# Performance work log

Measured on AMD Instinct MI355X. Metric: run time of the kernel, lower is better.

## Reference

```python
import jax, jax.numpy as jnp
import numpy as np
import math

B, SEQ, PRED, F, DM, NH, DFF, S, DMARK = 16, 336, 96, 7, 512, 8, 2048, 16, 5
EL, DL = 2, 1
DH = DM // NH


def _pe(max_len, d):
    pos = np.arange(max_len)[:, None].astype(np.float32)
    div = np.exp(np.arange(0, d, 2).astype(np.float32) * (-math.log(10000.0) / d))
    pe = np.zeros((max_len, d), np.float32)
    pe[:, 0::2] = np.sin(pos * div)
    pe[:, 1::2] = np.cos(pos * div)
    return jnp.asarray(pe)


def _make_tao():
    t = np.ones((S, S), np.float32)
    t[:, 0] = 0.0
    t[:, -1] = 0.0
    t[1] *= -1.0
    t[0] = 0.0
    t[0, 0] = 1.0
    t[2:, 1:-1] = np.eye(S - 2, dtype=np.float32)
    return jnp.asarray(t)


PE = _pe(2000, DM)
TAO = _make_tao()
ZVEC = jnp.zeros((S,), jnp.float32).at[:2].set(1.0)
MASK = jnp.triu(jnp.full((PRED, PRED), -1e9, jnp.float32), k=1)  # causal additive mask


def _ln(x, w, b, eps=1e-5):
    m = x.mean(-1, keepdims=True)
    v = ((x - m) ** 2).mean(-1, keepdims=True)
    return (x - m) * jax.lax.rsqrt(v + eps) * w + b


def _mha(q_in, kv_in, qkv_w, qkv_b, ow, ob, mask=None):
    wq, wk, wv = jnp.split(qkv_w, 3, axis=0)
    bq, bk, bv = jnp.split(qkv_b, 3, axis=0)

    def proj(x, w, bb):
        y = x @ w.T + bb  # [B, T, DM]
        return y.reshape(y.shape[0], y.shape[1], NH, DH).transpose(0, 2, 1, 3)

    q, k, v = proj(q_in, wq, bq), proj(kv_in, wk, bk), proj(kv_in, wv, bv)
    s = jnp.einsum('bhqd,bhkd->bhqk', q, k) / math.sqrt(DH)
    if mask is not None:
        s = s + mask
    a = jax.nn.softmax(s, axis=-1)
    o = jnp.einsum('bhqk,bhkd->bhqd', a, v)
    o = o.transpose(0, 2, 1, 3).reshape(q_in.shape)
    return o @ ow.T + ob


def _per_feature(xe, xd, eqw, eqb, eow, eob, el1w, el1b, el2w, el2b,
                 ef1w, ef1b, ef2w, ef2b, elw, elb,
                 dsqw, dsqb, dsow, dsob, dcqw, dcqb, dcow, dcob,
                 dl1w, dl1b, dl2w, dl2b, dl3w, dl3b, df1w, df1b, df2w, df2b):
    # post-norm TransformerEncoder (relu FFN), eval mode (no dropout)
    h = xe
    for l in range(EL):
        h = _ln(h + _mha(h, h, eqw[l], eqb[l], eow[l], eob[l]), el1w[l], el1b[l])
        ff = jax.nn.relu(h @ ef1w[l].T + ef1b[l]) @ ef2w[l].T + ef2b[l]
        h = _ln(h + ff, el2w[l], el2b[l])
    # encoder_linear maps time axis seqlen -> prelen
    mem = jnp.einsum('bsd,ps->bpd', h, elw) + elb[None, :, None]
    t = xd
    for l in range(DL):
        t = _ln(t + _mha(t, t, dsqw[l], dsqb[l], dsow[l], dsob[l], MASK), dl1w[l], dl1b[l])
        t = _ln(t + _mha(t, mem, dcqw[l], dcqb[l], dcow[l], dcob[l]), dl2w[l], dl2b[l])
        ff = jax.nn.relu(t @ df1w[l].T + df1b[l]) @ df2w[l].T + df2b[l]
        t = _ln(t + ff, dl3w[l], dl3b[l])
    return t


_vfeat = jax.vmap(_per_feature, in_axes=(1, 1) + (0,) * 32, out_axes=1)


def setup_inputs():
    key = jax.random.key(0)
    ks = iter(jax.random.split(key, 64))

    def rn(shape, s=0.05):
        return jax.random.normal(next(ks), shape, jnp.float32) * s

    return {
        'batch_x': rn((B, SEQ, F), 1.0),
        'batch_x_mark': rn((B, SEQ, DMARK - 1), 1.0),
        'batch_y': rn((B, PRED, F), 1.0),
        'batch_y_mark': rn((B, PRED, DMARK - 1), 1.0),
        'w_in': rn((DM, DMARK)), 'b_in': rn((DM,)),
        'w_co': rn((DM, DMARK - 1)), 'b_co': rn((DM,)),
        'eqw': rn((F, EL, 3 * DM, DM)), 'eqb': rn((F, EL, 3 * DM)),
        'eow': rn((F, EL, DM, DM)), 'eob': rn((F, EL, DM)),
        'el1w': jnp.ones((F, EL, DM)), 'el1b': jnp.zeros((F, EL, DM)),
        'el2w': jnp.ones((F, EL, DM)), 'el2b': jnp.zeros((F, EL, DM)),
        'ef1w': rn((F, EL, DFF, DM)), 'ef1b': rn((F, EL, DFF)),
        'ef2w': rn((F, EL, DM, DFF)), 'ef2b': rn((F, EL, DM)),
        'elw': rn((F, PRED, SEQ)), 'elb': rn((F, PRED)),
        'dsqw': rn((F, DL, 3 * DM, DM)), 'dsqb': rn((F, DL, 3 * DM)),
        'dsow': rn((F, DL, DM, DM)), 'dsob': rn((F, DL, DM)),
        'dcqw': rn((F, DL, 3 * DM, DM)), 'dcqb': rn((F, DL, 3 * DM)),
        'dcow': rn((F, DL, DM, DM)), 'dcob': rn((F, DL, DM)),
        'dl1w': jnp.ones((F, DL, DM)), 'dl1b': jnp.zeros((F, DL, DM)),
        'dl2w': jnp.ones((F, DL, DM)), 'dl2b': jnp.zeros((F, DL, DM)),
        'dl3w': jnp.ones((F, DL, DM)), 'dl3b': jnp.zeros((F, DL, DM)),
        'df1w': rn((F, DL, DFF, DM)), 'df1b': rn((F, DL, DFF)),
        'df2w': rn((F, DL, DM, DFF)), 'df2b': rn((F, DL, DM)),
        'wc': rn((S, DM)), 'bc': rn((S,)),
        'ws': rn((1, DM)), 'bs': rn((1,)),
    }


def reference(batch_x, batch_x_mark, batch_y, batch_y_mark,
              w_in, b_in, w_co, b_co,
              eqw, eqb, eow, eob, el1w, el1b, el2w, el2b,
              ef1w, ef1b, ef2w, ef2b, elw, elb,
              dsqw, dsqb, dsow, dsob, dcqw, dcqb, dcow, dcob,
              dl1w, dl1b, dl2w, dl2b, dl3w, dl3b, df1w, df1b, df2w, df2b,
              wc, bc, ws, bs):
    Bsz = batch_x.shape[0]
    # time marks are shared across features -> broadcast instead of concat loop
    hist = jnp.concatenate(
        [batch_x[..., None],
         jnp.broadcast_to(batch_x_mark[:, :, None, :], (Bsz, SEQ, F, DMARK - 1))], axis=-1)
    fut = jnp.broadcast_to(batch_y_mark[:, -PRED:, None, :], (Bsz, PRED, F, DMARK - 1))
    hist = hist.transpose(0, 2, 1, 3)  # [B, F, SEQ, DMARK]
    fut = fut.transpose(0, 2, 1, 3)    # [B, F, PRED, DMARK-1]
    xe = hist @ w_in.T + b_in + PE[:SEQ]
    xd = fut @ w_co.T + b_co + PE[:PRED]
    dec = _vfeat(xe, xd, eqw, eqb, eow, eob, el1w, el1b, el2w, el2b,
                 ef1w, ef1b, ef2w, ef2b, elw, elb,
                 dsqw, dsqb, dsow, dsob, dcqw, dcqb, dcow, dcob,
                 dl1w, dl1b, dl2w, dl2b, dl3w, dl3b, df1w, df1b, df2w, df2b)
    # g_c = Linear + Hardsigmoid; g_s = Linear + Softplus
    c = jnp.clip((jnp.einsum('bfpd,sd->bfps', dec, wc) + bc) / 6.0 + 0.5, 0.0, 1.0)
    sig = jax.nn.softplus(jnp.einsum('bfpd,d->bfp', dec, ws[0]) + bs[0])
    # linear state recurrence a = TAO @ a + c, y = z^T a, scanned over prediction days
    a0 = c[:, :, 0]                      # [B, F, S] (torch initializes a with day-0 g_c)
    cs = jnp.moveaxis(c, 2, 0)           # [PRED, B, F, S]
    ss = jnp.moveaxis(sig, 2, 0)         # [PRED, B, F]

    def step(a, xs):
        cd, sd = xs
        a = jnp.einsum('ij,bfj->bfi', TAO, a) + cd
        return a, jnp.einsum('s,bfs->bf', ZVEC, a) + sd

    _, ys = jax.lax.scan(step, a0, (cs, ss))
    return jnp.transpose(ys, (1, 0, 2))  # [B, PRED, F]
```

## Files before the change

kernel.cpp:

```cpp
#include <hip/hip_runtime.h>

typedef unsigned short u16;
typedef unsigned int   u32;
typedef __attribute__((ext_vector_type(8))) short short8;
typedef __attribute__((ext_vector_type(4))) float f32x4;

#define DEV static __device__ __forceinline__

DEV float bf2f(u16 u) { return __uint_as_float(((u32)u) << 16); }
DEV u16 f2bf(float f) {
  u32 u = __float_as_uint(f);
  return (u16)((u + 0x7fffu + ((u >> 16) & 1u)) >> 16);
}

#define GLD16(gp, lp) __builtin_amdgcn_global_load_lds( \
    (__attribute__((address_space(1))) u32*)(gp),       \
    (__attribute__((address_space(3))) u32*)(lp), 16, 0, 0)

__global__ __launch_bounds__(512, 2) void gemm_bf16(
    const u16* __restrict__ A, const u16* __restrict__ Bw, u16* __restrict__ C,
    const float* __restrict__ bias, int M, int N, int K,
    long sAz, long sBz, long sCz, long sBiasZ, int relu)
{
  __shared__ __align__(16) u16 Asm[2][256 * 64];
  __shared__ __align__(16) u16 Bsm[2][256 * 64];

  int gx = (int)gridDim.x, gy = (int)gridDim.y;
  int nwg = gx * gy * (int)gridDim.z;
  int orig = (int)blockIdx.x + gx * ((int)blockIdx.y + gy * (int)blockIdx.z);
  int q = nwg >> 3, r = nwg & 7;
  int xcd = orig & 7, pos = orig >> 3;
  int lg_id = (xcd < r) ? (xcd * (q + 1) + pos) : (r * (q + 1) + (xcd - r) * q + pos);
  int bz = lg_id / (gx * gy);
  int rem = lg_id - bz * (gx * gy);
  int by = rem / gx, bx = rem - by * gx;

  A += (size_t)bz * sAz; Bw += (size_t)bz * sBz; C += (size_t)bz * sCz; bias += (size_t)bz * sBiasZ;
  int tileM = bx * 256, tileN = by * 256;
  int tid = threadIdx.x, wave = tid >> 6, lane = tid & 63;
  int lr = lane & 15, lgp = lane >> 4;
  int wm = (wave >> 2) * 128;
  int wn = (wave & 3) * 64;

  const int NT = K >> 6;

  auto STAGE = [&](int b, int t) {
    int kb = t * 64;
    #pragma unroll
    for (int i = 0; i < 4; i++) {
      int gi = i * 512 + wave * 64 + lane;
      int row = gi >> 3, g = gi & 7;
      int gsw = (g ^ (row & 7)) * 8;
      GLD16(A + (size_t)(tileM + row) * K + kb + gsw, &Asm[b][(size_t)gi * 8]);
      GLD16(Bw + (size_t)(tileN + row) * K + kb + gsw, &Bsm[b][(size_t)gi * 8]);
    }
  };

  f32x4 acc[8][4] = {};

  STAGE(0, 0);
  if (NT > 1) STAGE(1, 1);

  for (int t = 0; t < NT; ++t) {
    int cur = t & 1;
    if (t + 1 < NT) asm volatile("s_waitcnt vmcnt(8)" ::: "memory");
    else            asm volatile("s_waitcnt vmcnt(0)" ::: "memory");
    asm volatile("s_barrier" ::: "memory");

    const u16* Ab = Asm[cur];
    const u16* Bb = Bsm[cur];
    #pragma unroll
    for (int ks = 0; ks < 2; ++ks) {
      short8 bfr[4], afr[8];
      #pragma unroll
      for (int n = 0; n < 4; ++n) {
        int row = wn + n * 16 + lr;
        bfr[n] = *(const short8*)(Bb + row * 64 + (((ks * 4 + lgp) ^ (row & 7)) * 8));
      }
      #pragma unroll
      for (int m = 0; m < 8; ++m) {
        int row = wm + m * 16 + lr;
        afr[m] = *(const short8*)(Ab + row * 64 + (((ks * 4 + lgp) ^ (row & 7)) * 8));
      }
      __builtin_amdgcn_s_setprio(1);
      #pragma unroll
      for (int m = 0; m < 8; ++m)
        #pragma unroll
        for (int n = 0; n < 4; ++n)
          acc[m][n] = __builtin_amdgcn_mfma_f32_16x16x32_bf16(afr[m], bfr[n], acc[m][n], 0, 0, 0);
      __builtin_amdgcn_s_setprio(0);
    }
    asm volatile("s_waitcnt lgkmcnt(0)" ::: "memory");
    asm volatile("s_barrier" ::: "memory");
    if (t + 2 < NT) STAGE(cur, t + 2);
  }

  #pragma unroll
  for (int n = 0; n < 4; ++n) {
    int ncol = tileN + wn + n * 16 + lr;
    float bb = bias[ncol];
    #pragma unroll
    for (int m = 0; m < 8; ++m) {
      int mrow = tileM + wm + m * 16 + lgp * 4;
      #pragma unroll
      for (int rr = 0; rr < 4; ++rr) {
        float v = acc[m][n][rr] + bb;
        if (relu) v = fmaxf(v, 0.f);
        C[(size_t)(mrow + rr) * N + ncol] = f2bf(v);
      }
    }
  }
}

__global__ void cvt_w_kernel(const float* __restrict__ src, u16* __restrict__ dst,
                             long n_per_f, long f_stride, long total4)
{
  long i = (long)blockIdx.x * blockDim.x + threadIdx.x;
  long step = (long)gridDim.x * blockDim.x;
  for (; i < total4; i += step) {
    long e = i * 4;
    long f = e / n_per_f; long r = e - f * n_per_f;
    float4 v = *(const float4*)(src + f * f_stride + r);
    *(ushort4*)(dst + e) = make_ushort4(f2bf(v.x), f2bf(v.y), f2bf(v.z), f2bf(v.w));
  }
}

__global__ __launch_bounds__(128) void embed_enc_k(
    const float* __restrict__ x, const float* __restrict__ mark,
    const float* __restrict__ w_in, const float* __restrict__ b_in,
    u16* __restrict__ hb)
{
  int row = blockIdx.x;
  int f = row / 5376; int rem = row - f * 5376; int b = rem / 336; int s = rem - b * 336;
  int bsix = b * 336 + s;
  float v0 = x[(size_t)bsix * 7 + f];
  float m0 = mark[(size_t)bsix * 4 + 0], m1 = mark[(size_t)bsix * 4 + 1];
  float m2 = mark[(size_t)bsix * 4 + 2], m3 = mark[(size_t)bsix * 4 + 3];
  int d0 = threadIdx.x * 4;
  u16 ob[4];
  #pragma unroll
  for (int c = 0; c < 4; c++) {
    int d = d0 + c;
    const float* w = w_in + d * 5;
    float val = w[0] * v0 + w[1] * m0 + w[2] * m1 + w[3] * m2 + w[4] * m3 + b_in[d];
    int i = d >> 1;
    float dv = expf((float)i * -0.0359778920778f);
    float arg = (float)s * dv;
    val += (d & 1) ? cosf(arg) : sinf(arg);
    ob[c] = f2bf(val);
  }
  *(ushort4*)(hb + (size_t)row * 512 + d0) = make_ushort4(ob[0], ob[1], ob[2], ob[3]);
}

__global__ __launch_bounds__(128) void embed_dec_k(
    const float* __restrict__ ymark, const float* __restrict__ w_co,
    const float* __restrict__ b_co, u16* __restrict__ tb)
{
  int row = blockIdx.x;
  int f = row / 1536; int rem = row - f * 1536; int b = rem / 96; int pp = rem - b * 96;
  int bp = b * 96 + pp;
  float m0 = ymark[(size_t)bp * 4 + 0], m1 = ymark[(size_t)bp * 4 + 1];
  float m2 = ymark[(size_t)bp * 4 + 2], m3 = ymark[(size_t)bp * 4 + 3];
  int d0 = threadIdx.x * 4;
  u16 ob[4];
  #pragma unroll
  for (int c = 0; c < 4; c++) {
    int d = d0 + c;
    const float* w = w_co + d * 4;
    float val = w[0] * m0 + w[1] * m1 + w[2] * m2 + w[3] * m3 + b_co[d];
    int i = d >> 1;
    float dv = expf((float)i * -0.0359778920778f);
    float arg = (float)pp * dv;
    val += (d & 1) ? cosf(arg) : sinf(arg);
    ob[c] = f2bf(val);
  }
  *(ushort4*)(tb + (size_t)row * 512 + d0) = make_ushort4(ob[0], ob[1], ob[2], ob[3]);
}

template<int LK>
__global__ __launch_bounds__(256) void attn_mfma(
    const u16* __restrict__ q, const u16* __restrict__ k, const u16* __restrict__ v,
    u16* __restrict__ out, int Lq, int qstride, int kvstride, int causal)
{
  constexpr int NKT = LK / 16;
  constexpr int NKS = (LK + 31) / 32;
  constexpr int KPAD = NKS * 32;
  constexpr int VSTR = 360;

  __shared__ __align__(16) u16 KsS[LK * 64];
  __shared__ __align__(16) u16 VtS[64 * VSTR];
  __shared__ __align__(16) u16 PWS[4][16 * VSTR];

  int hh = blockIdx.x, fb = blockIdx.y;
  int tid = threadIdx.x, wave = tid >> 6, lane = tid & 63;

  const u16* qp = q + (size_t)fb * Lq * qstride + hh * 64;
  const u16* kp = k + (size_t)fb * LK * kvstride + hh * 64;
  const u16* vp = v + (size_t)fb * LK * kvstride + hh * 64;

  {
    int r = (lane >> 3), s = lane & 7;
    for (int r0 = wave * 8; r0 < LK; r0 += 32) {
      int row = r0 + r;
      const u16* src = kp + (size_t)row * kvstride + ((s ^ (row & 7)) * 8);
      GLD16(src, KsS + r0 * 64 + lane * 8);
    }
  }
  for (int idx = tid; idx < LK * 8; idx += 256) {
    int kk = idx >> 3, dg = idx & 7;
    uint4 pv = *(const uint4*)(vp + (size_t)kk * kvstride + dg * 8);
    u16 e0 = (u16)pv.x, e1 = (u16)(pv.x >> 16);
    u16 e2 = (u16)pv.y, e3 = (u16)(pv.y >> 16);
    u16 e4 = (u16)pv.z, e5 = (u16)(pv.z >> 16);
    u16 e6 = (u16)pv.w, e7 = (u16)(pv.w >> 16);
    u16* col = VtS + (size_t)(dg * 8) * VSTR + kk;
    col[0 * VSTR] = e0; col[1 * VSTR] = e1; col[2 * VSTR] = e2; col[3 * VSTR] = e3;
    col[4 * VSTR] = e4; col[5 * VSTR] = e5; col[6 * VSTR] = e6; col[7 * VSTR] = e7;
  }
  if constexpr (KPAD > LK) {
    constexpr int TW = KPAD - LK;
    for (int i = tid; i < 64 * TW; i += 256)
      VtS[(i / TW) * VSTR + LK + (i % TW)] = 0;
    u16* PW = PWS[wave];
    for (int i = lane; i < 16 * TW; i += 64)
      PW[(i / TW) * VSTR + LK + (i % TW)] = 0;
  }
  __syncthreads();

  u16* PW = PWS[wave];
  int lr = lane & 15, lg = lane >> 4;
  int nqt = Lq / 16;

  for (int qt = wave; qt < nqt; qt += 4) {
    const u16* qrow = qp + (size_t)(qt * 16 + lr) * qstride + lg * 8;
    short8 qf0 = *(const short8*)(qrow);
    short8 qf1 = *(const short8*)(qrow + 32);

    f32x4 sacc[NKT];
    #pragma unroll
    for (int t = 0; t < NKT; t++) {
      int row = t * 16 + lr;
      const u16* kb = KsS + row * 64;
      short8 kf0 = *(const short8*)(kb + ((lg) ^ (row & 7)) * 8);
      short8 kf1 = *(const short8*)(kb + ((lg + 4) ^ (row & 7)) * 8);
      f32x4 s = {0.f, 0.f, 0.f, 0.f};
      s = __builtin_amdgcn_mfma_f32_16x16x32_bf16(qf0, kf0, s, 0, 0, 0);
      s = __builtin_amdgcn_mfma_f32_16x16x32_bf16(qf1, kf1, s, 0, 0, 0);
      sacc[t] = s;
    }

    float mx0 = -3e38f, mx1 = -3e38f, mx2 = -3e38f, mx3 = -3e38f;
    #pragma unroll
    for (int t = 0; t < NKT; t++) {
      int kg = t * 16 + lr;
      #pragma unroll
      for (int r = 0; r < 4; r++) {
        float val = sacc[t][r] * 0.125f;
        int qg = qt * 16 + lg * 4 + r;
        if (causal && kg > qg) val = -1e30f;
        sacc[t][r] = val;
        if (r == 0) mx0 = fmaxf(mx0, val);
        if (r == 1) mx1 = fmaxf(mx1, val);
        if (r == 2) mx2 = fmaxf(mx2, val);
        if (r == 3) mx3 = fmaxf(mx3, val);
      }
    }
    #pragma unroll
    for (int m = 1; m < 16; m <<= 1) {
      mx0 = fmaxf(mx0, __shfl_xor(mx0, m));
      mx1 = fmaxf(mx1, __shfl_xor(mx1, m));
      mx2 = fmaxf(mx2, __shfl_xor(mx2, m));
      mx3 = fmaxf(mx3, __shfl_xor(mx3, m));
    }
    float sm0 = 0.f, sm1 = 0.f, sm2 = 0.f, sm3 = 0.f;
    #pragma unroll
    for (int t = 0; t < NKT; t++) {
      float p0 = __expf(sacc[t][0] - mx0);
      float p1 = __expf(sacc[t][1] - mx1);
      float p2 = __expf(sacc[t][2] - mx2);
      float p3 = __expf(sacc[t][3] - mx3);
      sacc[t][0] = p0; sacc[t][1] = p1; sacc[t][2] = p2; sacc[t][3] = p3;
      sm0 += p0; sm1 += p1; sm2 += p2; sm3 += p3;
    }
    #pragma unroll
    for (int m = 1; m < 16; m <<= 1) {
      sm0 += __shfl_xor(sm0, m);
      sm1 += __shfl_xor(sm1, m);
      sm2 += __shfl_xor(sm2, m);
      sm3 += __shfl_xor(sm3, m);
    }
    float inv0 = 1.f / sm0, inv1 = 1.f / sm1, inv2 = 1.f / sm2, inv3 = 1.f / sm3;

    #pragma unroll
    for (int t = 0; t < NKT; t++) {
      u16* pw = PW + (size_t)(lg * 4) * VSTR + t * 16 + lr;
      pw[0 * VSTR] = f2bf(sacc[t][0]);
      pw[1 * VSTR] = f2bf(sacc[t][1]);
      pw[2 * VSTR] = f2bf(sacc[t][2]);
      pw[3 * VSTR] = f2bf(sacc[t][3]);
    }

    f32x4 oacc[4] = {};
    #pragma unroll
    for (int s = 0; s < NKS; s++) {
      short8 pf = *(const short8*)(PW + (size_t)lr * VSTR + s * 32 + lg * 8);
      #pragma unroll
      for (int j = 0; j < 4; j++) {
        short8 vf = *(const short8*)(VtS + (size_t)(j * 16 + lr) * VSTR + s * 32 + lg * 8);
        oacc[j] = __builtin_amdgcn_mfma_f32_16x16x32_bf16(pf, vf, oacc[j], 0, 0, 0);
      }
    }

    #pragma unroll
    for (int r = 0; r < 4; r++) {
      float inv = (r == 0) ? inv0 : (r == 1) ? inv1 : (r == 2) ? inv2 : inv3;
      size_t orow = (size_t)fb * Lq + qt * 16 + lg * 4 + r;
      u16* ob = out + orow * 512 + hh * 64 + lr;
      #pragma unroll
      for (int j = 0; j < 4; j++)
        ob[j * 16] = f2bf(oacc[j][r] * inv);
    }
  }
}

__global__ __launch_bounds__(128) void ln_kernel(
    u16* __restrict__ h, const u16* __restrict__ delta,
    const float* __restrict__ gamma, const float* __restrict__ beta,
    int rows_per_f, long gstride)
{
  __shared__ float red[2];
  int row = blockIdx.x;
  int f = row / rows_per_f;
  const float* g = gamma + (size_t)f * gstride;
  const float* be = beta + (size_t)f * gstride;
  int d0 = threadIdx.x * 4;
  size_t p = (size_t)row * 512 + d0;
  ushort4 hv = *(const ushort4*)(h + p);
  ushort4 dv = *(const ushort4*)(delta + p);
  float x0 = bf2f(hv.x) + bf2f(dv.x), x1 = bf2f(hv.y) + bf2f(dv.y);
  float x2 = bf2f(hv.z) + bf2f(dv.z), x3 = bf2f(hv.w) + bf2f(dv.w);
  float ssum = x0 + x1 + x2 + x3;
  #pragma unroll
  for (int m = 1; m < 64; m <<= 1) ssum += __shfl_xor(ssum, m);
  if ((threadIdx.x & 63) == 0) red[threadIdx.x >> 6] = ssum;
  __syncthreads();
  float mean = (red[0] + red[1]) * (1.f / 512.f);
  __syncthreads();
  float c0 = x0 - mean, c1 = x1 - mean, c2 = x2 - mean, c3 = x3 - mean;
  float sq = c0 * c0 + c1 * c1 + c2 * c2 + c3 * c3;
  #pragma unroll
  for (int m = 1; m < 64; m <<= 1) sq += __shfl_xor(sq, m);
  if ((threadIdx.x & 63) == 0) red[threadIdx.x >> 6] = sq;
  __syncthreads();
  float var = (red[0] + red[1]) * (1.f / 512.f);
  float rstd = rsqrtf(var + 1e-5f);
  float y0 = c0 * rstd * g[d0 + 0] + be[d0 + 0];
  float y1 = c1 * rstd * g[d0 + 1] + be[d0 + 1];
  float y2 = c2 * rstd * g[d0 + 2] + be[d0 + 2];
  float y3 = c3 * rstd * g[d0 + 3] + be[d0 + 3];
  *(ushort4*)(h + p) = make_ushort4(f2bf(y0), f2bf(y1), f2bf(y2), f2bf(y3));
}

__global__ __launch_bounds__(256) void mem_kernel(
    const u16* __restrict__ h, const float* __restrict__ elw,
    const float* __restrict__ elb, u16* __restrict__ memb)
{
  int fb = blockIdx.x; int f = fb >> 4;
  int pc = blockIdx.y;
  int d0 = threadIdx.x * 2;
  const u16* hbase = h + (size_t)fb * 336 * 512;
  const float* wbase = elw + (size_t)f * 96 * 336 + (size_t)pc * 16 * 336;
  float a0[16], a1[16];
  #pragma unroll
  for (int pp = 0; pp < 16; pp++) { a0[pp] = 0.f; a1[pp] = 0.f; }
  for (int s = 0; s < 336; s++) {
    ushort2 h2 = *(const ushort2*)(hbase + (size_t)s * 512 + d0);
    float hx = bf2f(h2.x), hy = bf2f(h2.y);
    #pragma unroll
    for (int pp = 0; pp < 16; pp++) {
      float w = wbase[pp * 336 + s];
      a0[pp] += w * hx; a1[pp] += w * hy;
    }
  }
  #pragma unroll
  for (int pp = 0; pp < 16; pp++) {
    int pidx = pc * 16 + pp;
    size_t row = (size_t)fb * 96 + pidx;
    float e = elb[f * 96 + pidx];
    *(ushort2*)(memb + row * 512 + d0) = make_ushort2(f2bf(a0[pp] + e), f2bf(a1[pp] + e));
  }
}

__global__ __launch_bounds__(64) void head_kernel(
    const u16* __restrict__ td, const float* __restrict__ wcp, const float* __restrict__ bcp,
    const float* __restrict__ wsp, const float* __restrict__ bsp,
    float* __restrict__ cb, float* __restrict__ sg, int f0)
{
  int rl = blockIdx.x, lane = threadIdx.x;
  size_t row = (size_t)f0 * 1536 + rl;
  const u16* x = td + (size_t)rl * 512;
  float xr[8];
  #pragma unroll
  for (int j = 0; j < 8; j++) xr[j] = bf2f(x[lane + 64 * j]);
  #pragma unroll
  for (int o = 0; o < 16; o++) {
    const float* w = wcp + o * 512;
    float p = 0.f;
    #pragma unroll
    for (int j = 0; j < 8; j++) p += xr[j] * w[lane + 64 * j];
    #pragma unroll
    for (int m = 1; m < 64; m <<= 1) p += __shfl_xor(p, m);
    if (lane == 0) {
      float cv = (p + bcp[o]) / 6.0f + 0.5f;
      cb[row * 16 + o] = fminf(fmaxf(cv, 0.f), 1.f);
    }
  }
  float p = 0.f;
  #pragma unroll
  for (int j = 0; j < 8; j++) p += xr[j] * wsp[lane + 64 * j];
  #pragma unroll
  for (int m = 1; m < 64; m <<= 1) p += __shfl_xor(p, m);
  if (lane == 0) {
    float zv = p + bsp[0];
    sg[row] = (zv > 20.f) ? zv : log1pf(expf(zv));
  }
}

__global__ __launch_bounds__(256) void scan_kernel(
    const float* __restrict__ cbuf, const float* __restrict__ sgb, float* __restrict__ outp)
{
  int f = blockIdx.x;
  int b = threadIdx.x >> 4;
  int s = threadIdx.x & 15;
  size_t rbase = ((size_t)f * 16 + b) * 96;
  float a = cbuf[rbase * 16 + s];
  for (int p = 0; p < 96; ++p) {
    float cd = cbuf[(rbase + p) * 16 + s];
    float sd = sgb[rbase + p];
    float xs = (s >= 1 && s <= 14) ? a : 0.f;
    #pragma unroll
    for (int m = 1; m < 16; m <<= 1) xs += __shfl_xor(xs, m);
    float up = __shfl_up(a, 1, 16);
    float an = (s == 0) ? (a + cd) : ((s == 1) ? (cd - xs) : (up + cd));
    a = an;
    float y01 = __shfl(a, 0, 16) + __shfl(a, 1, 16) + sd;
    if (s == 0) outp[((size_t)b * 96 + p) * 7 + f] = y01;
  }
}

__global__ void diag_kernel(float* __restrict__ out, float v, int n)
{
  int i = blockIdx.x * 256 + threadIdx.x;
  if (i < n) out[i] = v;
}

extern "C" void kernel_launch(void* const* d_in, const int* in_sizes, int n_in,
                              void* d_out, int out_size, void* d_ws, size_t ws_size,
                              hipStream_t stream)
{
  (void)in_sizes; (void)n_in;
  const float* batch_x      = (const float*)d_in[0];
  const float* batch_x_mark = (const float*)d_in[1];
  const float* batch_y_mark = (const float*)d_in[3];
  const float* w_in = (const float*)d_in[4];
  const float* b_in = (const float*)d_in[5];
  const float* w_co = (const float*)d_in[6];
  const float* b_co = (const float*)d_in[7];
  const float* eqw  = (const float*)d_in[8];
  const float* eqb  = (const float*)d_in[9];
  const float* eow  = (const float*)d_in[10];
  const float* eob  = (const float*)d_in[11];
  const float* el1w = (const float*)d_in[12];
  const float* el1b = (const float*)d_in[13];
  const float* el2w = (const float*)d_in[14];
  const float* el2b = (const float*)d_in[15];
  const float* ef1w = (const float*)d_in[16];
  const float* ef1b = (const float*)d_in[17];
  const float* ef2w = (const float*)d_in[18];
  const float* ef2b = (const float*)d_in[19];
  const float* elw  = (const float*)d_in[20];
  const float* elb  = (const float*)d_in[21];
  const float* dsqw = (const float*)d_in[22];
  const float* dsqb = (const float*)d_in[23];
  const float* dsow = (const float*)d_in[24];
  const float* dsob = (const float*)d_in[25];
  const float* dcqw = (const float*)d_in[26];
  const float* dcqb = (const float*)d_in[27];
  const float* dcow = (const float*)d_in[28];
  const float* dcob = (const float*)d_in[29];
  const float* dl1w = (const float*)d_in[30];
  const float* dl1b = (const float*)d_in[31];
  const float* dl2w = (const float*)d_in[32];
  const float* dl2b = (const float*)d_in[33];
  const float* dl3w = (const float*)d_in[34];
  const float* dl3b = (const float*)d_in[35];
  const float* df1w = (const float*)d_in[36];
  const float* df1b = (const float*)d_in[37];
  const float* df2w = (const float*)d_in[38];
  const float* df2b = (const float*)d_in[39];
  const float* wc   = (const float*)d_in[40];
  const float* bc   = (const float*)d_in[41];
  const float* wsg  = (const float*)d_in[42];
  const float* bsg  = (const float*)d_in[43];

  const size_t NE = 37632;
  const size_t ND = 10752;
  auto al = [](size_t x) { return (x + 255) & ~(size_t)255; };

  size_t fixedB = al(NE * 1024) + al(ND * 1024) + al(ND * 64) + al(ND * 4);
  int G = 0;
  for (int g = 7; g >= 1; --g) {
    size_t need = fixedB
        + al((size_t)g * 5376 * 2048 * 2)
        + al((size_t)g * 5376 * 512 * 2)
        + al((size_t)g * 2048 * 512 * 2)
        + al((size_t)g * 1536 * 512 * 2);
    if (need <= ws_size) { G = g; break; }
  }
  if (G == 0) {
    diag_kernel<<<dim3((out_size + 255) / 256), 256, 0, stream>>>(
        (float*)d_out, 1000.0f + (float)(ws_size >> 20), out_size);
    return;
  }

  char* base = (char*)d_ws;
  size_t off = 0;
  auto alloc = [&](size_t bytes) -> void* { void* r = base + off; off += al(bytes); return r; };
  u16*   hres = (u16*)  alloc(NE * 1024);
  u16*   tres = (u16*)  alloc(ND * 1024);
  float* cb   = (float*)alloc(ND * 64);
  float* sg   = (float*)alloc(ND * 4);
  u16*   bigc = (u16*)  alloc((size_t)G * 5376 * 2048 * 2);
  u16*   aobc = (u16*)  alloc((size_t)G * 5376 * 512 * 2);
  u16*   wbuf = (u16*)  alloc((size_t)G * 2048 * 512 * 2);
  u16*   memb = (u16*)  alloc((size_t)G * 1536 * 512 * 2);

  embed_enc_k<<<dim3(37632), 128, 0, stream>>>(batch_x, batch_x_mark, w_in, b_in, hres);
  embed_dec_k<<<dim3(10752), 128, 0, stream>>>(batch_y_mark, w_co, b_co, tres);

  auto cvtw = [&](const float* src, long n_per_f, long f_stride, int g) {
    cvt_w_kernel<<<dim3(512), 256, 0, stream>>>(src, wbuf, n_per_f, f_stride,
                                                (long)g * n_per_f / 4);
  };
  auto gemm = [&](const u16* A, long sAz, u16* C, long sCz, const float* bias, long sBias,
                  int M, int N, int K, int g, int relu) {
    dim3 gr(M / 256, N / 256, g);
    gemm_bf16<<<gr, 512, 0, stream>>>(A, wbuf, C, bias, M, N, K, sAz, (long)N * K, sCz,
                                      sBias, relu);
  };

  for (int f0 = 0; f0 < 7; f0 += G) {
    int g = (7 - f0 < G) ? (7 - f0) : G;
    u16* hc = hres + (size_t)f0 * 5376 * 512;
    u16* tc = tres + (size_t)f0 * 1536 * 512;

    for (int l = 0; l < 2; ++l) {
      cvtw(eqw + (size_t)f0 * 1572864 + (size_t)l * 786432, 786432L, 1572864L, g);
      gemm(hc, 5376L * 512, bigc, 5376L * 1536, eqb + f0 * 3072 + l * 1536, 3072,
           5376, 1536, 512, g, 0);
      attn_mfma<336><<<dim3(8, g * 16), 256, 0, stream>>>(
          bigc, bigc + 512, bigc + 1024, aobc, 336, 1536, 1536, 0);
      cvtw(eow + (size_t)f0 * 524288 + (size_t)l * 262144, 262144L, 524288L, g);
      gemm(aobc, 5376L * 512, bigc, 5376L * 512, eob + f0 * 1024 + l * 512, 1024,
           5376, 512, 512, g, 0);
      ln_kernel<<<dim3(g * 5376), 128, 0, stream>>>(
          hc, bigc, el1w + f0 * 1024 + l * 512, el1b + f0 * 1024 + l * 512, 5376, 1024);
      cvtw(ef1w + (size_t)f0 * 2097152 + (size_t)l * 1048576, 1048576L, 2097152L, g);
      gemm(hc, 5376L * 512, bigc, 5376L * 2048, ef1b + f0 * 4096 + l * 2048, 4096,
           5376, 2048, 512, g, 1);
      cvtw(ef2w + (size_t)f0 * 2097152 + (size_t)l * 1048576, 1048576L, 2097152L, g);
      gemm(bigc, 5376L * 2048, aobc, 5376L * 512, ef2b + f0 * 1024 + l * 512, 1024,
           5376, 512, 2048, g, 0);
      ln_kernel<<<dim3(g * 5376), 128, 0, stream>>>(
          hc, aobc, el2w + f0 * 1024 + l * 512, el2b + f0 * 1024 + l * 512, 5376, 1024);
    }

    mem_kernel<<<dim3(g * 16, 6), 256, 0, stream>>>(
        hc, elw + (size_t)f0 * 32256, elb + f0 * 96, memb);

    cvtw(dsqw + (size_t)f0 * 786432, 786432L, 786432L, g);
    gemm(tc, 1536L * 512, bigc, 1536L * 1536, dsqb + f0 * 1536, 1536,
         1536, 1536, 512, g, 0);
    attn_mfma<96><<<dim3(8, g * 16), 256, 0, stream>>>(
        bigc, bigc + 512, bigc + 1024, aobc, 96, 1536, 1536, 1);
    cvtw(dsow + (size_t)f0 * 262144, 262144L, 262144L, g);
    gemm(aobc, 1536L * 512, bigc, 1536L * 512, dsob + f0 * 512, 512,
         1536, 512, 512, g, 0);
    ln_kernel<<<dim3(g * 1536), 128, 0, stream>>>(
        tc, bigc, dl1w + f0 * 512, dl1b + f0 * 512, 1536, 512);

    cvtw(dcqw + (size_t)f0 * 786432, 262144L, 786432L, g);
    gemm(tc, 1536L * 512, bigc, 1536L * 512, dcqb + f0 * 1536, 1536,
         1536, 512, 512, g, 0);
    u16* bigKV = bigc + (size_t)g * 1536 * 512;
    cvtw(dcqw + (size_t)f0 * 786432 + 262144, 524288L, 786432L, g);
    gemm(memb, 1536L * 512, bigKV, 1536L * 1024, dcqb + f0 * 1536 + 512, 1536,
         1536, 1024, 512, g, 0);
    attn_mfma<96><<<dim3(8, g * 16), 256, 0, stream>>>(
        bigc, bigKV, bigKV + 512, aobc, 96, 512, 1024, 0);
    cvtw(dcow + (size_t)f0 * 262144, 262144L, 262144L, g);
    gemm(aobc, 1536L * 512, bigc, 1536L * 512, dcob + f0 * 512, 512,
         1536, 512, 512, g, 0);
    ln_kernel<<<dim3(g * 1536), 128, 0, stream>>>(
        tc, bigc, dl2w + f0 * 512, dl2b + f0 * 512, 1536, 512);

    cvtw(df1w + (size_t)f0 * 1048576, 1048576L, 1048576L, g);
    gemm(tc, 1536L * 512, bigc, 1536L * 2048, df1b + f0 * 2048, 2048,
         1536, 2048, 512, g, 1);
    cvtw(df2w + (size_t)f0 * 1048576, 1048576L, 1048576L, g);
    gemm(bigc, 1536L * 2048, aobc, 1536L * 512, df2b + f0 * 512, 512,
         1536, 512, 2048, g, 0);
    ln_kernel<<<dim3(g * 1536), 128, 0, stream>>>(
        tc, aobc, dl3w + f0 * 512, dl3b + f0 * 512, 1536, 512);

    head_kernel<<<dim3(g * 1536), 64, 0, stream>>>(tc, wc, bc, wsg, bsg, cb, sg, f0);
  }

  scan_kernel<<<dim3(7), 256, 0, stream>>>(cb, sg, (float*)d_out);
}
```

Before: 1.766 ms.

## Chunk K/V in attention kernel and drop max-subtraction in softmax

Result: faster. 1.695 ms (-4.0%).

```diff
diff --git a/kernel.cpp b/kernel.cpp
--- a/kernel.cpp
+++ b/kernel.cpp
@@ -177,148 +177,137 @@
   *(ushort4*)(tb + (size_t)row * 512 + d0) = make_ushort4(ob[0], ob[1], ob[2], ob[3]);
 }
 
-template<int LK>
+template<int LK, int CHUNK, int NQI>
 __global__ __launch_bounds__(256) void attn_mfma(
     const u16* __restrict__ q, const u16* __restrict__ k, const u16* __restrict__ v,
     u16* __restrict__ out, int Lq, int qstride, int kvstride, int causal)
 {
-  constexpr int NKT = LK / 16;
-  constexpr int NKS = (LK + 31) / 32;
+  constexpr int NCH = LK / CHUNK;
+  constexpr int NKT = CHUNK / 16;
+  constexpr int NKS = (CHUNK + 31) / 32;
   constexpr int KPAD = NKS * 32;
-  constexpr int VSTR = 360;
-
-  __shared__ __align__(16) u16 KsS[LK * 64];
+  constexpr int VSTR = KPAD + 8;
+  constexpr int NGRP = CHUNK * 8 / 64;
+
+  __shared__ __align__(16) u16 KsS[CHUNK * 64];
   __shared__ __align__(16) u16 VtS[64 * VSTR];
   __shared__ __align__(16) u16 PWS[4][16 * VSTR];
 
   int hh = blockIdx.x, fb = blockIdx.y;
   int tid = threadIdx.x, wave = tid >> 6, lane = tid & 63;
+  int lr = lane & 15, lg = lane >> 4;
 
   const u16* qp = q + (size_t)fb * Lq * qstride + hh * 64;
   const u16* kp = k + (size_t)fb * LK * kvstride + hh * 64;
   const u16* vp = v + (size_t)fb * LK * kvstride + hh * 64;
 
-  {
-    int r = (lane >> 3), s = lane & 7;
-    for (int r0 = wave * 8; r0 < LK; r0 += 32) {
-      int row = r0 + r;
-      const u16* src = kp + (size_t)row * kvstride + ((s ^ (row & 7)) * 8);
-      GLD16(src, KsS + r0 * 64 + lane * 8);
-    }
-  }
-  for (int idx = tid; idx < LK * 8; idx += 256) {
-    int kk = idx >> 3, dg = idx & 7;
-    uint4 pv = *(const uint4*)(vp + (size_t)kk * kvstride + dg * 8);
-    u16 e0 = (u16)pv.x, e1 = (u16)(pv.x >> 16);
-    u16 e2 = (u16)pv.y, e3 = (u16)(pv.y >> 16);
-    u16 e4 = (u16)pv.z, e5 = (u16)(pv.z >> 16);
-    u16 e6 = (u16)pv.w, e7 = (u16)(pv.w >> 16);
-    u16* col = VtS + (size_t)(dg * 8) * VSTR + kk;
-    col[0 * VSTR] = e0; col[1 * VSTR] = e1; col[2 * VSTR] = e2; col[3 * VSTR] = e3;
-    col[4 * VSTR] = e4; col[5 * VSTR] = e5; col[6 * VSTR] = e6; col[7 * VSTR] = e7;
-  }
-  if constexpr (KPAD > LK) {
-    constexpr int TW = KPAD - LK;
+  if constexpr (KPAD > CHUNK) {
+    constexpr int TW = KPAD - CHUNK;
     for (int i = tid; i < 64 * TW; i += 256)
-      VtS[(i / TW) * VSTR + LK + (i % TW)] = 0;
+      VtS[(i / TW) * VSTR + CHUNK + (i % TW)] = 0;
     u16* PW = PWS[wave];
     for (int i = lane; i < 16 * TW; i += 64)
-      PW[(i / TW) * VSTR + LK + (i % TW)] = 0;
-  }
-  __syncthreads();
-
+      PW[(i / TW) * VSTR + CHUNK + (i % TW)] = 0;
+  }
+
+  f32x4 oacc[NQI][4] = {};
+  f32x4 lsum[NQI] = {};
+  const int nqt = Lq / 16;
   u16* PW = PWS[wave];
-  int lr = lane & 15, lg = lane >> 4;
-  int nqt = Lq / 16;
-
-  for (int qt = wave; qt < nqt; qt += 4) {
-    const u16* qrow = qp + (size_t)(qt * 16 + lr) * qstride + lg * 8;
-    short8 qf0 = *(const short8*)(qrow);
-    short8 qf1 = *(const short8*)(qrow + 32);
-
-    f32x4 sacc[NKT];
-    #pragma unroll
-    for (int t = 0; t < NKT; t++) {
-      int row = t * 16 + lr;
-      const u16* kb = KsS + row * 64;
-      short8 kf0 = *(const short8*)(kb + ((lg) ^ (row & 7)) * 8);
-      short8 kf1 = *(const short8*)(kb + ((lg + 4) ^ (row & 7)) * 8);
-      f32x4 s = {0.f, 0.f, 0.f, 0.f};
-      s = __builtin_amdgcn_mfma_f32_16x16x32_bf16(qf0, kf0, s, 0, 0, 0);
-      s = __builtin_amdgcn_mfma_f32_16x16x32_bf16(qf1, kf1, s, 0, 0, 0);
-      sacc[t] = s;
-    }
-
-    float mx0 = -3e38f, mx1 = -3e38f, mx2 = -3e38f, mx3 = -3e38f;
-    #pragma unroll
-    for (int t = 0; t < NKT; t++) {
-      int kg = t * 16 + lr;
+
+  for (int c = 0; c < NCH; ++c) {
+    __syncthreads();
+
+    const u16* kcp = kp + (size_t)c * CHUNK * kvstride;
+    for (int grp = wave; grp < NGRP; grp += 4) {
+      int gi = grp * 64 + lane;
+      int row = gi >> 3, g = gi & 7;
+      GLD16(kcp + (size_t)row * kvstride + ((g ^ (row & 7)) * 8), KsS + (size_t)gi * 8);
+    }
+    const u16* vcp = vp + (size_t)c * CHUNK * kvstride;
+    for (int idx = tid; idx < CHUNK * 8; idx += 256) {
+      int kk = idx >> 3, dg = idx & 7;
+      uint4 pv = *(const uint4*)(vcp + (size_t)kk * kvstride + dg * 8);
+      u16* col = VtS + (size_t)(dg * 8) * VSTR + kk;
+      col[0 * VSTR] = (u16)pv.x; col[1 * VSTR] = (u16)(pv.x >> 16);
+      col[2 * VSTR] = (u16)pv.y; col[3 * VSTR] = (u16)(pv.y >> 16);
+      col[4 * VSTR] = (u16)pv.z; col[5 * VSTR] = (u16)(pv.z >> 16);
+      col[6 * VSTR] = (u16)pv.w; col[7 * VSTR] = (u16)(pv.w >> 16);
+    }
+    __syncthreads();
+
+    #pragma unroll
+    for (int qi = 0; qi < NQI; ++qi) {
+      int qt = wave + qi * 4;
+      if (qt < nqt) {
+        const u16* qrow = qp + (size_t)(qt * 16 + lr) * qstride + lg * 8;
+        short8 qf0 = *(const short8*)(qrow);
+        short8 qf1 = *(const short8*)(qrow + 32);
+
+        f32x4 sacc[NKT];
+        #pragma unroll
+        for (int t = 0; t < NKT; t++) {
+          int row = t * 16 + lr;
+          const u16* kb = KsS + row * 64;
+          short8 kf0 = *(const short8*)(kb + ((lg ^ (row & 7)) * 8));
+          short8 kf1 = *(const short8*)(kb + (((lg + 4) ^ (row & 7)) * 8));
+          f32x4 s = {0.f, 0.f, 0.f, 0.f};
+          s = __builtin_amdgcn_mfma_f32_16x16x32_bf16(qf0, kf0, s, 0, 0, 0);
+          s = __builtin_amdgcn_mfma_f32_16x16x32_bf16(qf1, kf1, s, 0, 0, 0);
+          sacc[t] = s;
+        }
+
+        #pragma unroll
+        for (int t = 0; t < NKT; t++) {
+          int kg = c * CHUNK + t * 16 + lr;
+          #pragma unroll
+          for (int r = 0; r < 4; r++) {
+            int qg = qt * 16 + lg * 4 + r;
+            float p = (causal && kg > qg) ? 0.f : __expf(sacc[t][r] * 0.125f);
+            sacc[t][r] = p;
+            lsum[qi][r] += p;
+          }
+          u16* pw = PW + (size_t)(lg * 4) * VSTR + t * 16 + lr;
+          pw[0 * VSTR] = f2bf(sacc[t][0]);
+          pw[1 * VSTR] = f2bf(sacc[t][1]);
+          pw[2 * VSTR] = f2bf(sacc[t][2]);
+          pw[3 * VSTR] = f2bf(sacc[t][3]);
+        }
+
+        #pragma unroll
+        for (int s = 0; s < NKS; s++) {
+          short8 pf = *(const short8*)(PW + (size_t)lr * VSTR + s * 32 + lg * 8);
+          #pragma unroll
+          for (int j = 0; j < 4; j++) {
+            short8 vf = *(const short8*)(VtS + (size_t)(j * 16 + lr) * VSTR + s * 32 + lg * 8);
+            oacc[qi][j] = __builtin_amdgcn_mfma_f32_16x16x32_bf16(pf, vf, oacc[qi][j], 0, 0, 0);
+          }
+        }
+      }
+    }
+  }
+
+  #pragma unroll
+  for (int qi = 0; qi < NQI; ++qi) {
+    int qt = wave + qi * 4;
+    if (qt < nqt) {
+      float l0 = lsum[qi][0], l1 = lsum[qi][1], l2 = lsum[qi][2], l3 = lsum[qi][3];
+      #pragma unroll
+      for (int m = 1; m < 16; m <<= 1) {
+        l0 += __shfl_xor(l0, m);
+        l1 += __shfl_xor(l1, m);
+        l2 += __shfl_xor(l2, m);
+        l3 += __shfl_xor(l3, m);
+      }
+      float inv[4] = {1.f / l0, 1.f / l1, 1.f / l2, 1.f / l3};
       #pragma unroll
       for (int r = 0; r < 4; r++) {
-        float val = sacc[t][r] * 0.125f;
-        int qg = qt * 16 + lg * 4 + r;
-        if (causal && kg > qg) val = -1e30f;
-        sacc[t][r] = val;
-        if (r == 0) mx0 = fmaxf(mx0, val);
-        if (r == 1) mx1 = fmaxf(mx1, val);
-        if (r == 2) mx2 = fmaxf(mx2, val);
-        if (r == 3) mx3 = fmaxf(mx3, val);
+        size_t orow = (size_t)fb * Lq + qt * 16 + lg * 4 + r;
+        u16* ob = out + orow * 512 + hh * 64 + lr;
+        #pragma unroll
+        for (int j = 0; j < 4; j++)
+          ob[j * 16] = f2bf(oacc[qi][j][r] * inv[r]);
       }
-    }
-    #pragma unroll
-    for (int m = 1; m < 16; m <<= 1) {
-      mx0 = fmaxf(mx0, __shfl_xor(mx0, m));
-      mx1 = fmaxf(mx1, __shfl_xor(mx1, m));
-      mx2 = fmaxf(mx2, __shfl_xor(mx2, m));
-      mx3 = fmaxf(mx3, __shfl_xor(mx3, m));
-    }
-    float sm0 = 0.f, sm1 = 0.f, sm2 = 0.f, sm3 = 0.f;
-    #pragma unroll
-    for (int t = 0; t < NKT; t++) {
-      float p0 = __expf(sacc[t][0] - mx0);
-      float p1 = __expf(sacc[t][1] - mx1);
-      float p2 = __expf(sacc[t][2] - mx2);
-      float p3 = __expf(sacc[t][3] - mx3);
-      sacc[t][0] = p0; sacc[t][1] = p1; sacc[t][2] = p2; sacc[t][3] = p3;
-      sm0 += p0; sm1 += p1; sm2 += p2; sm3 += p3;
-    }
-    #pragma unroll
-    for (int m = 1; m < 16; m <<= 1) {
-      sm0 += __shfl_xor(sm0, m);
-      sm1 += __shfl_xor(sm1, m);
-      sm2 += __shfl_xor(sm2, m);
-      sm3 += __shfl_xor(sm3, m);
-    }
-    float inv0 = 1.f / sm0, inv1 = 1.f / sm1, inv2 = 1.f / sm2, inv3 = 1.f / sm3;
-
-    #pragma unroll
-    for (int t = 0; t < NKT; t++) {
-      u16* pw = PW + (size_t)(lg * 4) * VSTR + t * 16 + lr;
-      pw[0 * VSTR] = f2bf(sacc[t][0]);
-      pw[1 * VSTR] = f2bf(sacc[t][1]);
-      pw[2 * VSTR] = f2bf(sacc[t][2]);
-      pw[3 * VSTR] = f2bf(sacc[t][3]);
-    }
-
-    f32x4 oacc[4] = {};
-    #pragma unroll
-    for (int s = 0; s < NKS; s++) {
-      short8 pf = *(const short8*)(PW + (size_t)lr * VSTR + s * 32 + lg * 8);
-      #pragma unroll
-      for (int j = 0; j < 4; j++) {
-        short8 vf = *(const short8*)(VtS + (size_t)(j * 16 + lr) * VSTR + s * 32 + lg * 8);
-        oacc[j] = __builtin_amdgcn_mfma_f32_16x16x32_bf16(pf, vf, oacc[j], 0, 0, 0);
-      }
-    }
-
-    #pragma unroll
-    for (int r = 0; r < 4; r++) {
-      float inv = (r == 0) ? inv0 : (r == 1) ? inv1 : (r == 2) ? inv2 : inv3;
-      size_t orow = (size_t)fb * Lq + qt * 16 + lg * 4 + r;
-      u16* ob = out + orow * 512 + hh * 64 + lr;
-      #pragma unroll
-      for (int j = 0; j < 4; j++)
-        ob[j * 16] = f2bf(oacc[j][r] * inv);
     }
   }
 }
@@ -558,7 +547,7 @@
       cvtw(eqw + (size_t)f0 * 1572864 + (size_t)l * 786432, 786432L, 1572864L, g);
       gemm(hc, 5376L * 512, bigc, 5376L * 1536, eqb + f0 * 3072 + l * 1536, 3072,
            5376, 1536, 512, g, 0);
-      attn_mfma<336><<<dim3(8, g * 16), 256, 0, stream>>>(
+      attn_mfma<336, 112, 6><<<dim3(8, g * 16), 256, 0, stream>>>(
           bigc, bigc + 512, bigc + 1024, aobc, 336, 1536, 1536, 0);
       cvtw(eow + (size_t)f0 * 524288 + (size_t)l * 262144, 262144L, 524288L, g);
       gemm(aobc, 5376L * 512, bigc, 5376L * 512, eob + f0 * 1024 + l * 512, 1024,
@@ -581,7 +570,7 @@
     cvtw(dsqw + (size_t)f0 * 786432, 786432L, 786432L, g);
     gemm(tc, 1536L * 512, bigc, 1536L * 1536, dsqb + f0 * 1536, 1536,
          1536, 1536, 512, g, 0);
-    attn_mfma<96><<<dim3(8, g * 16), 256, 0, stream>>>(
+    attn_mfma<96, 96, 2><<<dim3(8, g * 16), 256, 0, stream>>>(
         bigc, bigc + 512, bigc + 1024, aobc, 96, 1536, 1536, 1);
     cvtw(dsow + (size_t)f0 * 262144, 262144L, 262144L, g);
     gemm(aobc, 1536L * 512, bigc, 1536L * 512, dsob + f0 * 512, 512,
@@ -596,7 +585,7 @@
     cvtw(dcqw + (size_t)f0 * 786432 + 262144, 524288L, 786432L, g);
     gemm(memb, 1536L * 512, bigKV, 1536L * 1024, dcqb + f0 * 1536 + 512, 1536,
          1536, 1024, 512, g, 0);
-    attn_mfma<96><<<dim3(8, g * 16), 256, 0, stream>>>(
+    attn_mfma<96, 96, 2><<<dim3(8, g * 16), 256, 0, stream>>>(
         bigc, bigKV, bigKV + 512, aobc, 96, 512, 1024, 0);
     cvtw(dcow + (size_t)f0 * 262144, 262144L, 262144L, g);
     gemm(aobc, 1536L * 512, bigc, 1536L * 512, dcob + f0 * 512, 512,
```
